# Kernel tuning notes

Hardware: AMD Instinct MI355X
Metric: run time of the kernel (lower is better)

The kernel has to match this reference:

```python
import jax, jax.numpy as jnp
import numpy as np

H, C = 2, 128  # heads, per-head channels
NEG_SLOPE = 0.2

N_FACT, N_STATUTE, N_CHARGE = 50000, 2000, 200
D_FACT, D_STATUTE, D_CHARGE = 768, 256, 128
E_M, E_I = 500000, 20000
NUM_CHARGES = 10


def setup_inputs() -> dict:
    key = jax.random.key(0)
    ks = iter(jax.random.split(key, 64))
    d = {}
    d['x_fact'] = jax.random.normal(next(ks), (N_FACT, D_FACT), jnp.float32)
    d['x_statute'] = jax.random.normal(next(ks), (N_STATUTE, D_STATUTE), jnp.float32)
    d['x_charge'] = jax.random.normal(next(ks), (N_CHARGE, D_CHARGE), jnp.float32)

    def gat_params(d_src, d_dst):
        s = 1.0 / np.sqrt(max(d_src, 1))
        return (jax.random.normal(next(ks), (d_src, H * C), jnp.float32) * s,
                jax.random.normal(next(ks), (d_dst, H * C), jnp.float32) * (1.0 / np.sqrt(d_dst)),
                jax.random.normal(next(ks), (H, C), jnp.float32) * 0.1,
                jax.random.normal(next(ks), (H, C), jnp.float32) * 0.1,
                jnp.zeros((H * C,), jnp.float32))
    # relation params: m = fact->statute, rm = statute->fact, i = statute->charge, ri = charge->statute
    (d['Wsrc_m'], d['Wdst_m'], d['asrc_m'], d['adst_m'], d['b_m']) = gat_params(D_FACT, D_STATUTE)
    (d['Wsrc_rm'], d['Wdst_rm'], d['asrc_rm'], d['adst_rm'], d['b_rm']) = gat_params(D_STATUTE, D_FACT)
    (d['Wsrc_i'], d['Wdst_i'], d['asrc_i'], d['adst_i'], d['b_i']) = gat_params(D_STATUTE, D_CHARGE)
    (d['Wsrc_ri'], d['Wdst_ri'], d['asrc_ri'], d['adst_ri'], d['b_ri']) = gat_params(D_CHARGE, D_STATUTE)
    d['Wc'] = jax.random.normal(next(ks), (H * C, NUM_CHARGES), jnp.float32) * (1.0 / np.sqrt(H * C))
    d['bc'] = jnp.zeros((NUM_CHARGES,), jnp.float32)

    d['m_src'] = jax.random.randint(next(ks), (E_M,), 0, N_FACT, jnp.int32)
    d['m_dst'] = jax.random.randint(next(ks), (E_M,), 0, N_STATUTE, jnp.int32)
    d['rm_src'] = jax.random.randint(next(ks), (E_M,), 0, N_STATUTE, jnp.int32)
    d['rm_dst'] = jax.random.randint(next(ks), (E_M,), 0, N_FACT, jnp.int32)
    d['i_src'] = jax.random.randint(next(ks), (E_I,), 0, N_STATUTE, jnp.int32)
    d['i_dst'] = jax.random.randint(next(ks), (E_I,), 0, N_CHARGE, jnp.int32)
    d['ri_src'] = jax.random.randint(next(ks), (E_I,), 0, N_CHARGE, jnp.int32)
    d['ri_dst'] = jax.random.randint(next(ks), (E_I,), 0, N_STATUTE, jnp.int32)
    return d


def gat_conv(xs, xd, Wsrc, Wdst, asrc, adst, bias, src, dst, n_dst):
    # bipartite GATConv, heads=2, concat=True, add_self_loops=False
    hs = (xs @ Wsrc).reshape(-1, H, C)          # [Ns,H,C]
    hd = (xd @ Wdst).reshape(-1, H, C)          # [Nd,H,C]
    als = jnp.einsum('nhc,hc->nh', hs, asrc)    # [Ns,H]
    ald = jnp.einsum('nhc,hc->nh', hd, adst)    # [Nd,H]
    e = jax.nn.leaky_relu(als[src] + ald[dst], NEG_SLOPE)  # [E,H]
    mx = jax.ops.segment_max(e, dst, num_segments=n_dst)
    ex = jnp.exp(e - mx[dst])
    denom = jax.ops.segment_sum(ex, dst, num_segments=n_dst)
    alpha = ex / (denom[dst] + 1e-16)           # segment softmax over dst groups
    msg = alpha[:, :, None] * hs[src]           # [E,H,C]
    out = jax.ops.segment_sum(msg, dst, num_segments=n_dst)
    return out.reshape(n_dst, H * C) + bias


def reference(x_fact, x_statute, x_charge,
              Wsrc_m, Wdst_m, asrc_m, adst_m, b_m,
              Wsrc_rm, Wdst_rm, asrc_rm, adst_rm, b_rm,
              Wsrc_i, Wdst_i, asrc_i, adst_i, b_i,
              Wsrc_ri, Wdst_ri, asrc_ri, adst_ri, b_ri,
              Wc, bc,
              m_src, m_dst, rm_src, rm_dst, i_src, i_dst, ri_src, ri_dst):
    out_st_m = gat_conv(x_fact, x_statute, Wsrc_m, Wdst_m, asrc_m, adst_m, b_m, m_src, m_dst, N_STATUTE)
    out_st_ri = gat_conv(x_charge, x_statute, Wsrc_ri, Wdst_ri, asrc_ri, adst_ri, b_ri, ri_src, ri_dst, N_STATUTE)
    statute_emb = 0.5 * (out_st_m + out_st_ri)  # HeteroConv aggr='mean' (unused downstream)
    fact_emb = gat_conv(x_statute, x_fact, Wsrc_rm, Wdst_rm, asrc_rm, adst_rm, b_rm, rm_src, rm_dst, N_FACT)
    charge_emb = gat_conv(x_statute, x_charge, Wsrc_i, Wdst_i, asrc_i, adst_i, b_i, i_src, i_dst, N_CHARGE)
    del statute_emb, charge_emb  # computed by the module but not used by classifier
    return fact_emb @ Wc + bc    # [N_FACT, NUM_CHARGES]
```

## Files before the change

### kernel.cpp

```cpp
#include <hip/hip_runtime.h>
#include <math.h>

#define NFACT 50000
#define NST   2000
#define DFACT 768
#define HC    256
#define EM    500000
#define NK    10
#define NEG   0.2f

#define SCAN_B 196

__device__ __forceinline__ float lrelu(float x) { return x > 0.f ? x : NEG * x; }

__global__ __launch_bounds__(256) void k_hs(const float* __restrict__ xs,
                                            const float* __restrict__ Wsrc,
                                            const float* __restrict__ asrc,
                                            const float* __restrict__ Wc,
                                            float* __restrict__ als,
                                            float* __restrict__ hsW) {
    int s = blockIdx.x, t = threadIdx.x;
    __shared__ float xrow[256];
    __shared__ float hrow[256];
    __shared__ float wsum[4];
    xrow[t] = xs[s * 256 + t];
    __syncthreads();
    float acc = 0.f;
    for (int d = 0; d < 256; ++d) acc += xrow[d] * Wsrc[d * 256 + t];
    float p = acc * asrc[t];
    for (int o = 32; o; o >>= 1) p += __shfl_xor(p, o, 64);
    hrow[t] = acc;
    if ((t & 63) == 0) wsum[t >> 6] = p;
    __syncthreads();
    if (t < 20) {
        int h = t / 10, k = t - h * 10;
        float a = 0.f;
        int base = h * 128;
        for (int c = 0; c < 128; ++c) a += hrow[base + c] * Wc[(base + c) * NK + k];
        hsW[s * 20 + t] = a;
    }
    if (t == 0) { als[s * 2 + 0] = wsum[0] + wsum[1]; als[s * 2 + 1] = wsum[2] + wsum[3]; }
}

__global__ __launch_bounds__(256) void k_v(const float* __restrict__ Wdst,
                                           const float* __restrict__ adst,
                                           float* __restrict__ V) {
    int t = blockIdx.x * 256 + threadIdx.x;
    if (t >= DFACT * 2) return;
    int d = t >> 1, h = t & 1;
    float acc = 0.f;
    for (int c = 0; c < 128; ++c)
        acc += Wdst[d * 256 + h * 128 + c] * adst[h * 128 + c];
    V[d * 2 + h] = acc;
}

__global__ void k_cst(const float* __restrict__ b_rm, const float* __restrict__ Wc,
                      const float* __restrict__ bc, float* __restrict__ cst) {
    int k = threadIdx.x;
    if (k < NK) {
        float a = bc[k];
        for (int ch = 0; ch < HC; ++ch) a += b_rm[ch] * Wc[ch * NK + k];
        cst[k] = a;
    }
}

__global__ __launch_bounds__(256) void k_ald(const float* __restrict__ xf,
                                             const float* __restrict__ V,
                                             float* __restrict__ ald) {
    int lane = threadIdx.x & 63, wid = threadIdx.x >> 6;
    int n = blockIdx.x * 4 + wid;
    const float* row = xf + (size_t)n * DFACT;
    float a0 = 0.f, a1 = 0.f;
    #pragma unroll
    for (int r = 0; r < 3; ++r) {
        int j0 = r * 256 + lane * 4;
        const float4 u = *(const float4*)(row + j0);
        a0 += u.x * V[(j0 + 0) * 2 + 0] + u.y * V[(j0 + 1) * 2 + 0]
            + u.z * V[(j0 + 2) * 2 + 0] + u.w * V[(j0 + 3) * 2 + 0];
        a1 += u.x * V[(j0 + 0) * 2 + 1] + u.y * V[(j0 + 1) * 2 + 1]
            + u.z * V[(j0 + 2) * 2 + 1] + u.w * V[(j0 + 3) * 2 + 1];
    }
    for (int o = 32; o; o >>= 1) { a0 += __shfl_xor(a0, o, 64); a1 += __shfl_xor(a1, o, 64); }
    if (lane == 0) { ald[n * 2 + 0] = a0; ald[n * 2 + 1] = a1; }
}

__global__ void k_zero(int* __restrict__ p, int n) {
    int i = blockIdx.x * 256 + threadIdx.x;
    if (i < n) p[i] = 0;
}
__global__ void k_hist(const int* __restrict__ dst, int* __restrict__ counts) {
    int e = blockIdx.x * 256 + threadIdx.x;
    if (e < EM) atomicAdd(&counts[dst[e]], 1);
}

__global__ __launch_bounds__(256) void k_scanA(const int* __restrict__ counts,
                                               int* __restrict__ bsum) {
    __shared__ int sd[256];
    int t = threadIdx.x, i = blockIdx.x * 256 + t;
    int c = (i <= NFACT) ? counts[i] : 0;
    int v = c;
    for (int o = 32; o; o >>= 1) v += __shfl_xor(v, o, 64);
    if ((t & 63) == 0) sd[t >> 6] = v;
    __syncthreads();
    if (t == 0) bsum[blockIdx.x] = sd[0] + sd[1] + sd[2] + sd[3];
}
__global__ __launch_bounds__(256) void k_scanB(const int* __restrict__ bsum,
                                               int* __restrict__ boff) {
    __shared__ int sd[256];
    int t = threadIdx.x;
    sd[t] = (t < SCAN_B) ? bsum[t] : 0;
    __syncthreads();
    for (int o = 1; o < 256; o <<= 1) {
        int v = (t >= o) ? sd[t - o] : 0;
        __syncthreads();
        sd[t] += v;
        __syncthreads();
    }
    if (t < SCAN_B) boff[t] = (t > 0) ? sd[t - 1] : 0;
}
__global__ __launch_bounds__(256) void k_scanC(const int* __restrict__ counts,
                                               const int* __restrict__ boff,
                                               int* __restrict__ offs,
                                               int* __restrict__ cursor) {
    __shared__ int sd[256];
    int t = threadIdx.x, i = blockIdx.x * 256 + t;
    int c = (i <= NFACT) ? counts[i] : 0;
    sd[t] = c;
    __syncthreads();
    for (int o = 1; o < 256; o <<= 1) {
        int v = (t >= o) ? sd[t - o] : 0;
        __syncthreads();
        sd[t] += v;
        __syncthreads();
    }
    if (i <= NFACT) {
        int excl = boff[blockIdx.x] + sd[t] - c;
        offs[i] = excl;
        cursor[i] = excl;
    }
}

__global__ void k_scatw(const int* __restrict__ src, const int* __restrict__ dst,
                        const float2* __restrict__ als2, const float2* __restrict__ ald2,
                        int* __restrict__ cursor,
                        int* __restrict__ perm_s, float2* __restrict__ perm_w) {
    int e = blockIdx.x * 256 + threadIdx.x;
    if (e >= EM) return;
    int s = src[e], d = dst[e];
    float2 a  = als2[s];
    float2 al = ald2[d];
    float w0 = __expf(lrelu(a.x + al.x));
    float w1 = __expf(lrelu(a.y + al.y));
    int pos = atomicAdd(&cursor[d], 1);
    perm_s[pos] = s;
    perm_w[pos] = make_float2(w0, w1);
}

__global__ __launch_bounds__(256) void k_agg(const float* __restrict__ hsW,
                                             const int* __restrict__ offs,
                                             const int* __restrict__ perm_s,
                                             const float2* __restrict__ perm_w,
                                             const float* __restrict__ cst,
                                             float* __restrict__ out) {
    int lane = threadIdx.x & 63, wid = threadIdx.x >> 6;
    int n = blockIdx.x * 4 + wid;
    int beg = offs[n], end = offs[n + 1];
    bool live = lane < 20;
    bool h0   = lane < 10;

    float acc = 0.f, d0 = 0.f, d1 = 0.f;
    int j = beg;
    for (; j + 4 <= end; j += 4) {
        int sA = perm_s[j + 0], sB = perm_s[j + 1], sC = perm_s[j + 2], sD = perm_s[j + 3];
        float2 wA = perm_w[j + 0], wB = perm_w[j + 1], wC = perm_w[j + 2], wD = perm_w[j + 3];
        float hA = live ? hsW[sA * 20 + lane] : 0.f;
        float hB = live ? hsW[sB * 20 + lane] : 0.f;
        float hC = live ? hsW[sC * 20 + lane] : 0.f;
        float hD = live ? hsW[sD * 20 + lane] : 0.f;
        d0 += wA.x + wB.x + wC.x + wD.x;
        d1 += wA.y + wB.y + wC.y + wD.y;
        acc += (h0 ? wA.x : wA.y) * hA + (h0 ? wB.x : wB.y) * hB
             + (h0 ? wC.x : wC.y) * hC + (h0 ? wD.x : wD.y) * hD;
    }
    for (; j < end; ++j) {
        int s = perm_s[j];
        float2 w = perm_w[j];
        float h = live ? hsW[s * 20 + lane] : 0.f;
        d0 += w.x; d1 += w.y;
        acc += (h0 ? w.x : w.y) * h;
    }
    float dh = h0 ? d0 : d1;
    float r = acc / (dh + 1e-16f);
    float other = __shfl(r, (lane + 10) & 63, 64);
    if (h0) out[n * NK + lane] = r + other + cst[lane];
}

__global__ void k_sentinel(float* __restrict__ out, int n, float val) {
    int i = blockIdx.x * 256 + threadIdx.x;
    if (i < n) out[i] = val;
}

extern "C" void kernel_launch(void* const* d_in, const int* in_sizes, int n_in,
                              void* d_out, int out_size, void* d_ws, size_t ws_size,
                              hipStream_t stream) {
    const float* x_fact    = (const float*)d_in[0];
    const float* x_statute = (const float*)d_in[1];
    const float* Wsrc_rm   = (const float*)d_in[8];
    const float* Wdst_rm   = (const float*)d_in[9];
    const float* asrc_rm   = (const float*)d_in[10];
    const float* adst_rm   = (const float*)d_in[11];
    const float* b_rm      = (const float*)d_in[12];
    const float* Wc        = (const float*)d_in[23];
    const float* bc        = (const float*)d_in[24];
    const int* rm_src      = (const int*)d_in[27];
    const int* rm_dst      = (const int*)d_in[28];
    float* out = (float*)d_out;

    char* w0p = (char*)d_ws;
    char* w = w0p;
    auto carve = [&](size_t bytes) -> void* {
        void* p = (void*)w;
        w += (bytes + 511) & ~(size_t)511;
        return p;
    };
    float*  als    = (float*)carve((size_t)NST * 2 * 4);
    float*  hsW    = (float*)carve((size_t)NST * 20 * 4);
    float*  V      = (float*)carve((size_t)DFACT * 2 * 4);
    float*  ald    = (float*)carve((size_t)NFACT * 2 * 4);
    float*  cst    = (float*)carve(64);
    int*    counts = (int*)carve((size_t)(NFACT + 1) * 4);
    int*    offs   = (int*)carve((size_t)(NFACT + 1) * 4);
    int*    cursor = (int*)carve((size_t)(NFACT + 1) * 4);
    int*    bsum   = (int*)carve((size_t)SCAN_B * 4);
    int*    boff   = (int*)carve((size_t)SCAN_B * 4);
    int*    perm_s = (int*)carve((size_t)EM * 4);
    float2* perm_w = (float2*)carve((size_t)EM * 8);
    if ((size_t)(w - w0p) > ws_size) {
        k_sentinel<<<(out_size + 255) / 256, 256, 0, stream>>>(out, out_size, 2000.f);
        return;
    }

    k_zero<<<(NFACT + 256) / 256, 256, 0, stream>>>(counts, NFACT + 1);
    k_hs<<<NST, 256, 0, stream>>>(x_statute, Wsrc_rm, asrc_rm, Wc, als, hsW);
    k_v<<<(DFACT * 2 + 255) / 256, 256, 0, stream>>>(Wdst_rm, adst_rm, V);
    k_cst<<<1, 64, 0, stream>>>(b_rm, Wc, bc, cst);
    k_ald<<<NFACT / 4, 256, 0, stream>>>(x_fact, V, ald);
    k_hist<<<(EM + 255) / 256, 256, 0, stream>>>(rm_dst, counts);
    k_scanA<<<SCAN_B, 256, 0, stream>>>(counts, bsum);
    k_scanB<<<1, 256, 0, stream>>>(bsum, boff);
    k_scanC<<<SCAN_B, 256, 0, stream>>>(counts, boff, offs, cursor);
    k_scatw<<<(EM + 255) / 256, 256, 0, stream>>>(rm_src, rm_dst,
                                                  (const float2*)als, (const float2*)ald,
                                                  cursor, perm_s, perm_w);
    k_agg<<<NFACT / 4, 256, 0, stream>>>(hsW, offs, perm_s, perm_w, cst, out);
}
```

Baseline: 415.2 us.

## Fuse prep kernels, use block-local shared histogram/scatter, recompute attention weights in aggregation

Merges the statute projection, V, and constant kernels into one launch. It co-schedules the fact-side attention dot with a histogram in which each block scans all edges and counts only its own 256-node destination range using shared atomics. The three scan kernels become one, with each block redundantly scanning the block sums. The scatter now uses shared-memory cursors and writes only source indices, and edge weights are recomputed inside the aggregation instead of being stored. This removes the global atomics, the zeroing pass and the weight buffer traffic, at the cost of each of the 196 blocks rereading the whole destination array twice.

```diff
diff --git a/kernel.cpp b/kernel.cpp
--- a/kernel.cpp
+++ b/kernel.cpp
@@ -8,122 +8,124 @@
 #define EM    500000
 #define NK    10
 #define NEG   0.2f
-
-#define SCAN_B 196
+#define NHB   196
 
 __device__ __forceinline__ float lrelu(float x) { return x > 0.f ? x : NEG * x; }
 
-__global__ __launch_bounds__(256) void k_hs(const float* __restrict__ xs,
-                                            const float* __restrict__ Wsrc,
-                                            const float* __restrict__ asrc,
-                                            const float* __restrict__ Wc,
-                                            float* __restrict__ als,
-                                            float* __restrict__ hsW) {
-    int s = blockIdx.x, t = threadIdx.x;
-    __shared__ float xrow[256];
-    __shared__ float hrow[256];
-    __shared__ float wsum[4];
-    xrow[t] = xs[s * 256 + t];
-    __syncthreads();
-    float acc = 0.f;
-    for (int d = 0; d < 256; ++d) acc += xrow[d] * Wsrc[d * 256 + t];
-    float p = acc * asrc[t];
-    for (int o = 32; o; o >>= 1) p += __shfl_xor(p, o, 64);
-    hrow[t] = acc;
-    if ((t & 63) == 0) wsum[t >> 6] = p;
-    __syncthreads();
-    if (t < 20) {
-        int h = t / 10, k = t - h * 10;
-        float a = 0.f;
-        int base = h * 128;
-        for (int c = 0; c < 128; ++c) a += hrow[base + c] * Wc[(base + c) * NK + k];
-        hsW[s * 20 + t] = a;
-    }
-    if (t == 0) { als[s * 2 + 0] = wsum[0] + wsum[1]; als[s * 2 + 1] = wsum[2] + wsum[3]; }
-}
-
-__global__ __launch_bounds__(256) void k_v(const float* __restrict__ Wdst,
-                                           const float* __restrict__ adst,
-                                           float* __restrict__ V) {
-    int t = blockIdx.x * 256 + threadIdx.x;
-    if (t >= DFACT * 2) return;
-    int d = t >> 1, h = t & 1;
-    float acc = 0.f;
-    for (int c = 0; c < 128; ++c)
-        acc += Wdst[d * 256 + h * 128 + c] * adst[h * 128 + c];
-    V[d * 2 + h] = acc;
-}
-
-__global__ void k_cst(const float* __restrict__ b_rm, const float* __restrict__ Wc,
-                      const float* __restrict__ bc, float* __restrict__ cst) {
-    int k = threadIdx.x;
-    if (k < NK) {
-        float a = bc[k];
-        for (int ch = 0; ch < HC; ++ch) a += b_rm[ch] * Wc[ch * NK + k];
-        cst[k] = a;
-    }
-}
-
-__global__ __launch_bounds__(256) void k_ald(const float* __restrict__ xf,
-                                             const float* __restrict__ V,
-                                             float* __restrict__ ald) {
-    int lane = threadIdx.x & 63, wid = threadIdx.x >> 6;
-    int n = blockIdx.x * 4 + wid;
-    const float* row = xf + (size_t)n * DFACT;
-    float a0 = 0.f, a1 = 0.f;
-    #pragma unroll
-    for (int r = 0; r < 3; ++r) {
-        int j0 = r * 256 + lane * 4;
-        const float4 u = *(const float4*)(row + j0);
-        a0 += u.x * V[(j0 + 0) * 2 + 0] + u.y * V[(j0 + 1) * 2 + 0]
-            + u.z * V[(j0 + 2) * 2 + 0] + u.w * V[(j0 + 3) * 2 + 0];
-        a1 += u.x * V[(j0 + 0) * 2 + 1] + u.y * V[(j0 + 1) * 2 + 1]
-            + u.z * V[(j0 + 2) * 2 + 1] + u.w * V[(j0 + 3) * 2 + 1];
-    }
-    for (int o = 32; o; o >>= 1) { a0 += __shfl_xor(a0, o, 64); a1 += __shfl_xor(a1, o, 64); }
-    if (lane == 0) { ald[n * 2 + 0] = a0; ald[n * 2 + 1] = a1; }
-}
-
-__global__ void k_zero(int* __restrict__ p, int n) {
-    int i = blockIdx.x * 256 + threadIdx.x;
-    if (i < n) p[i] = 0;
-}
-__global__ void k_hist(const int* __restrict__ dst, int* __restrict__ counts) {
-    int e = blockIdx.x * 256 + threadIdx.x;
-    if (e < EM) atomicAdd(&counts[dst[e]], 1);
-}
-
-__global__ __launch_bounds__(256) void k_scanA(const int* __restrict__ counts,
-                                               int* __restrict__ bsum) {
+__global__ __launch_bounds__(256) void k_prep(const float* __restrict__ xs,
+                                              const float* __restrict__ Wsrc,
+                                              const float* __restrict__ asrc,
+                                              const float* __restrict__ Wc,
+                                              const float* __restrict__ Wdst,
+                                              const float* __restrict__ adst,
+                                              const float* __restrict__ b_rm,
+                                              const float* __restrict__ bc,
+                                              float* __restrict__ als,
+                                              float* __restrict__ hsW,
+                                              float* __restrict__ V,
+                                              float* __restrict__ cst) {
+    int b = blockIdx.x, t = threadIdx.x;
+    if (b < NST) {
+        __shared__ float xrow[256];
+        __shared__ float hrow[256];
+        __shared__ float wsum[4];
+        xrow[t] = xs[b * 256 + t];
+        __syncthreads();
+        float acc = 0.f;
+        for (int d = 0; d < 256; ++d) acc += xrow[d] * Wsrc[d * 256 + t];
+        float p = acc * asrc[t];
+        for (int o = 32; o; o >>= 1) p += __shfl_xor(p, o, 64);
+        hrow[t] = acc;
+        if ((t & 63) == 0) wsum[t >> 6] = p;
+        __syncthreads();
+        if (t < 20) {
+            int h = t / 10, k = t - h * 10;
+            float a = 0.f;
+            int base = h * 128;
+            for (int c = 0; c < 128; ++c) a += hrow[base + c] * Wc[(base + c) * NK + k];
+            hsW[b * 20 + t] = a;
+        }
+        if (t == 0) { als[b * 2 + 0] = wsum[0] + wsum[1]; als[b * 2 + 1] = wsum[2] + wsum[3]; }
+    } else if (b < NST + 6) {
+        int i = (b - NST) * 256 + t;
+        if (i < DFACT * 2) {
+            int d = i >> 1, h = i & 1;
+            float acc = 0.f;
+            for (int c = 0; c < 128; ++c)
+                acc += Wdst[d * 256 + h * 128 + c] * adst[h * 128 + c];
+            V[d * 2 + h] = acc;
+        }
+    } else {
+        if (t < NK) {
+            float a = bc[t];
+            for (int ch = 0; ch < HC; ++ch) a += b_rm[ch] * Wc[ch * NK + t];
+            cst[t] = a;
+        }
+    }
+}
+
+__global__ __launch_bounds__(1024) void k_ald_hist(const float* __restrict__ xf,
+                                                   const float* __restrict__ V,
+                                                   const int* __restrict__ dst,
+                                                   float* __restrict__ ald,
+                                                   int* __restrict__ counts,
+                                                   int* __restrict__ bsum) {
+    int b = blockIdx.x, t = threadIdx.x;
+    if (b < NHB) {
+        __shared__ int hcnt[256];
+        __shared__ int hsum[4];
+        if (t < 256) hcnt[t] = 0;
+        __syncthreads();
+        int base = b << 8;
+        for (int e = t; e < EM; e += 1024) {
+            unsigned local = (unsigned)(dst[e] - base);
+            if (local < 256u) atomicAdd(&hcnt[local], 1);
+        }
+        __syncthreads();
+        if (t < 256) {
+            int idx = base + t;
+            if (idx <= NFACT) counts[idx] = hcnt[t];
+            int v = hcnt[t];
+            for (int o = 32; o; o >>= 1) v += __shfl_xor(v, o, 64);
+            if ((t & 63) == 0) hsum[t >> 6] = v;
+        }
+        __syncthreads();
+        if (t == 0) bsum[b] = hsum[0] + hsum[1] + hsum[2] + hsum[3];
+    } else {
+        int lane = t & 63, wid = t >> 6;
+        int n = (b - NHB) * 16 + wid;
+        const float* row = xf + (size_t)n * DFACT;
+        float a0 = 0.f, a1 = 0.f;
+        #pragma unroll
+        for (int r = 0; r < 3; ++r) {
+            int j0 = r * 256 + lane * 4;
+            const float4 u = *(const float4*)(row + j0);
+            a0 += u.x * V[(j0 + 0) * 2 + 0] + u.y * V[(j0 + 1) * 2 + 0]
+                + u.z * V[(j0 + 2) * 2 + 0] + u.w * V[(j0 + 3) * 2 + 0];
+            a1 += u.x * V[(j0 + 0) * 2 + 1] + u.y * V[(j0 + 1) * 2 + 1]
+                + u.z * V[(j0 + 2) * 2 + 1] + u.w * V[(j0 + 3) * 2 + 1];
+        }
+        for (int o = 32; o; o >>= 1) { a0 += __shfl_xor(a0, o, 64); a1 += __shfl_xor(a1, o, 64); }
+        if (lane == 0) { ald[n * 2 + 0] = a0; ald[n * 2 + 1] = a1; }
+    }
+}
+
+__global__ __launch_bounds__(256) void k_scan(const int* __restrict__ counts,
+                                              const int* __restrict__ bsum,
+                                              int* __restrict__ offs) {
+    __shared__ int sb[256];
     __shared__ int sd[256];
-    int t = threadIdx.x, i = blockIdx.x * 256 + t;
-    int c = (i <= NFACT) ? counts[i] : 0;
-    int v = c;
-    for (int o = 32; o; o >>= 1) v += __shfl_xor(v, o, 64);
-    if ((t & 63) == 0) sd[t >> 6] = v;
-    __syncthreads();
-    if (t == 0) bsum[blockIdx.x] = sd[0] + sd[1] + sd[2] + sd[3];
-}
-__global__ __launch_bounds__(256) void k_scanB(const int* __restrict__ bsum,
-                                               int* __restrict__ boff) {
-    __shared__ int sd[256];
-    int t = threadIdx.x;
-    sd[t] = (t < SCAN_B) ? bsum[t] : 0;
+    int t = threadIdx.x, b = blockIdx.x;
+    sb[t] = (t < NHB) ? bsum[t] : 0;
     __syncthreads();
     for (int o = 1; o < 256; o <<= 1) {
-        int v = (t >= o) ? sd[t - o] : 0;
-        __syncthreads();
-        sd[t] += v;
-        __syncthreads();
-    }
-    if (t < SCAN_B) boff[t] = (t > 0) ? sd[t - 1] : 0;
-}
-__global__ __launch_bounds__(256) void k_scanC(const int* __restrict__ counts,
-                                               const int* __restrict__ boff,
-                                               int* __restrict__ offs,
-                                               int* __restrict__ cursor) {
-    __shared__ int sd[256];
-    int t = threadIdx.x, i = blockIdx.x * 256 + t;
+        int v = (t >= o) ? sb[t - o] : 0;
+        __syncthreads();
+        sb[t] += v;
+        __syncthreads();
+    }
+    int myoff = (b > 0) ? sb[b - 1] : 0;
+    int i = b * 256 + t;
     int c = (i <= NFACT) ? counts[i] : 0;
     sd[t] = c;
     __syncthreads();
@@ -133,33 +135,36 @@
         sd[t] += v;
         __syncthreads();
     }
-    if (i <= NFACT) {
-        int excl = boff[blockIdx.x] + sd[t] - c;
-        offs[i] = excl;
-        cursor[i] = excl;
-    }
-}
-
-__global__ void k_scatw(const int* __restrict__ src, const int* __restrict__ dst,
-                        const float2* __restrict__ als2, const float2* __restrict__ ald2,
-                        int* __restrict__ cursor,
-                        int* __restrict__ perm_s, float2* __restrict__ perm_w) {
-    int e = blockIdx.x * 256 + threadIdx.x;
-    if (e >= EM) return;
-    int s = src[e], d = dst[e];
-    float2 a  = als2[s];
-    float2 al = ald2[d];
-    float w0 = __expf(lrelu(a.x + al.x));
-    float w1 = __expf(lrelu(a.y + al.y));
-    int pos = atomicAdd(&cursor[d], 1);
-    perm_s[pos] = s;
-    perm_w[pos] = make_float2(w0, w1);
+    if (i <= NFACT) offs[i] = myoff + sd[t] - c;
+}
+
+__global__ __launch_bounds__(1024) void k_scat(const int* __restrict__ src,
+                                               const int* __restrict__ dst,
+                                               const int* __restrict__ offs,
+                                               int* __restrict__ perm_s) {
+    __shared__ int cur[256];
+    int b = blockIdx.x, t = threadIdx.x;
+    int base = b << 8;
+    if (t < 256) {
+        int i = base + t;
+        cur[t] = (i <= NFACT) ? offs[i] : 0;
+    }
+    __syncthreads();
+    for (int e = t; e < EM; e += 1024) {
+        int d = dst[e];
+        unsigned local = (unsigned)(d - base);
+        if (local < 256u) {
+            int p = atomicAdd(&cur[local], 1);
+            perm_s[p] = src[e];
+        }
+    }
 }
 
 __global__ __launch_bounds__(256) void k_agg(const float* __restrict__ hsW,
                                              const int* __restrict__ offs,
                                              const int* __restrict__ perm_s,
-                                             const float2* __restrict__ perm_w,
+                                             const float2* __restrict__ als2,
+                                             const float2* __restrict__ ald2,
                                              const float* __restrict__ cst,
                                              float* __restrict__ out) {
     int lane = threadIdx.x & 63, wid = threadIdx.x >> 6;
@@ -167,30 +172,34 @@
     int beg = offs[n], end = offs[n + 1];
     bool live = lane < 20;
     bool h0   = lane < 10;
-
-    float acc = 0.f, d0 = 0.f, d1 = 0.f;
+    float2 aldn = ald2[n];
+    float al = h0 ? aldn.x : aldn.y;
+
+    float acc = 0.f, den = 0.f;
     int j = beg;
     for (; j + 4 <= end; j += 4) {
         int sA = perm_s[j + 0], sB = perm_s[j + 1], sC = perm_s[j + 2], sD = perm_s[j + 3];
-        float2 wA = perm_w[j + 0], wB = perm_w[j + 1], wC = perm_w[j + 2], wD = perm_w[j + 3];
+        float2 aA = als2[sA], aB = als2[sB], aC = als2[sC], aD = als2[sD];
         float hA = live ? hsW[sA * 20 + lane] : 0.f;
         float hB = live ? hsW[sB * 20 + lane] : 0.f;
         float hC = live ? hsW[sC * 20 + lane] : 0.f;
         float hD = live ? hsW[sD * 20 + lane] : 0.f;
-        d0 += wA.x + wB.x + wC.x + wD.x;
-        d1 += wA.y + wB.y + wC.y + wD.y;
-        acc += (h0 ? wA.x : wA.y) * hA + (h0 ? wB.x : wB.y) * hB
-             + (h0 ? wC.x : wC.y) * hC + (h0 ? wD.x : wD.y) * hD;
+        float wA = __expf(lrelu((h0 ? aA.x : aA.y) + al));
+        float wB = __expf(lrelu((h0 ? aB.x : aB.y) + al));
+        float wC = __expf(lrelu((h0 ? aC.x : aC.y) + al));
+        float wD = __expf(lrelu((h0 ? aD.x : aD.y) + al));
+        den += (wA + wB) + (wC + wD);
+        acc += wA * hA + wB * hB + wC * hC + wD * hD;
     }
     for (; j < end; ++j) {
         int s = perm_s[j];
-        float2 w = perm_w[j];
+        float2 a = als2[s];
         float h = live ? hsW[s * 20 + lane] : 0.f;
-        d0 += w.x; d1 += w.y;
-        acc += (h0 ? w.x : w.y) * h;
-    }
-    float dh = h0 ? d0 : d1;
-    float r = acc / (dh + 1e-16f);
+        float w = __expf(lrelu((h0 ? a.x : a.y) + al));
+        den += w;
+        acc += w * h;
+    }
+    float r = acc / (den + 1e-16f);
     float other = __shfl(r, (lane + 10) & 63, 64);
     if (h0) out[n * NK + lane] = r + other + cst[lane];
 }
@@ -223,34 +232,26 @@
         w += (bytes + 511) & ~(size_t)511;
         return p;
     };
-    float*  als    = (float*)carve((size_t)NST * 2 * 4);
-    float*  hsW    = (float*)carve((size_t)NST * 20 * 4);
-    float*  V      = (float*)carve((size_t)DFACT * 2 * 4);
-    float*  ald    = (float*)carve((size_t)NFACT * 2 * 4);
-    float*  cst    = (float*)carve(64);
-    int*    counts = (int*)carve((size_t)(NFACT + 1) * 4);
-    int*    offs   = (int*)carve((size_t)(NFACT + 1) * 4);
-    int*    cursor = (int*)carve((size_t)(NFACT + 1) * 4);
-    int*    bsum   = (int*)carve((size_t)SCAN_B * 4);
-    int*    boff   = (int*)carve((size_t)SCAN_B * 4);
-    int*    perm_s = (int*)carve((size_t)EM * 4);
-    float2* perm_w = (float2*)carve((size_t)EM * 8);
+    float* als    = (float*)carve((size_t)NST * 2 * 4);
+    float* hsW    = (float*)carve((size_t)NST * 20 * 4);
+    float* V      = (float*)carve((size_t)DFACT * 2 * 4);
+    float* ald    = (float*)carve((size_t)NFACT * 2 * 4);
+    float* cst    = (float*)carve(64);
+    int*   counts = (int*)carve((size_t)(NFACT + 1) * 4);
+    int*   offs   = (int*)carve((size_t)(NFACT + 1) * 4);
+    int*   bsum   = (int*)carve((size_t)NHB * 4);
+    int*   perm_s = (int*)carve((size_t)EM * 4);
     if ((size_t)(w - w0p) > ws_size) {
         k_sentinel<<<(out_size + 255) / 256, 256, 0, stream>>>(out, out_size, 2000.f);
         return;
     }
 
-    k_zero<<<(NFACT + 256) / 256, 256, 0, stream>>>(counts, NFACT + 1);
-    k_hs<<<NST, 256, 0, stream>>>(x_statute, Wsrc_rm, asrc_rm, Wc, als, hsW);
-    k_v<<<(DFACT * 2 + 255) / 256, 256, 0, stream>>>(Wdst_rm, adst_rm, V);
-    k_cst<<<1, 64, 0, stream>>>(b_rm, Wc, bc, cst);
-    k_ald<<<NFACT / 4, 256, 0, stream>>>(x_fact, V, ald);
-    k_hist<<<(EM + 255) / 256, 256, 0, stream>>>(rm_dst, counts);
-    k_scanA<<<SCAN_B, 256, 0, stream>>>(counts, bsum);
-    k_scanB<<<1, 256, 0, stream>>>(bsum, boff);
-    k_scanC<<<SCAN_B, 256, 0, stream>>>(counts, boff, offs, cursor);
-    k_scatw<<<(EM + 255) / 256, 256, 0, stream>>>(rm_src, rm_dst,
-                                                  (const float2*)als, (const float2*)ald,
-                                                  cursor, perm_s, perm_w);
-    k_agg<<<NFACT / 4, 256, 0, stream>>>(hsW, offs, perm_s, perm_w, cst, out);
-}
+    k_prep<<<NST + 7, 256, 0, stream>>>(x_statute, Wsrc_rm, asrc_rm, Wc,
+                                        Wdst_rm, adst_rm, b_rm, bc,
+                                        als, hsW, V, cst);
+    k_ald_hist<<<NHB + NFACT / 16, 1024, 0, stream>>>(x_fact, V, rm_dst, ald, counts, bsum);
+    k_scan<<<NHB, 256, 0, stream>>>(counts, bsum, offs);
+    k_scat<<<NHB, 1024, 0, stream>>>(rm_src, rm_dst, offs, perm_s);
+    k_agg<<<NFACT / 4, 256, 0, stream>>>(hsW, offs, perm_s,
+                                         (const float2*)als, (const float2*)ald, cst, out);
+}
```

New measurement: 670.4 us. 61.5% more time.
